# Kernel optimization log

Measured on AMD Instinct MI355X. Metric: run time of the kernel, lower is better.

Reference implementation:

```python
import jax, jax.numpy as jnp
import numpy as np


def _shared_mlp(x, W, s, b):
    # 1x1 conv over channel dim (last axis) + folded BN (scale/shift) + ReLU
    # x: (..., Cin), W: (Cout, Cin), s/b: (Cout,)
    return jax.nn.relu(jnp.einsum('...c,oc->...o', x, W) * s + b)


def setup_inputs() -> dict:
    key = jax.random.key(0)
    ks = jax.random.split(key, 15)
    B, N, K, C = 4, 4096, 32, 64
    D1, D2, DH = 64, 64, 128
    sc = 0.1
    return {
        'xyz': jax.random.normal(ks[0], (B, N, 3), dtype=jnp.float32),
        'features': jax.random.normal(ks[1], (B, C, N), dtype=jnp.float32),
        'idx': jax.random.randint(ks[2], (N, K), 0, N, dtype=jnp.int32),
        'W_gu': jax.random.normal(ks[3], (D1, 6), dtype=jnp.float32) * sc,
        's_gu': jnp.ones((D1,), jnp.float32),
        'b_gu': jax.random.normal(ks[4], (D1,), dtype=jnp.float32) * sc,
        'W_gv': jax.random.normal(ks[5], (D2, C), dtype=jnp.float32) * sc,
        's_gv': jnp.ones((D2,), jnp.float32),
        'b_gv': jax.random.normal(ks[6], (D2,), dtype=jnp.float32) * sc,
        'W_h': jax.random.normal(ks[7], (DH, D1 + D2), dtype=jnp.float32) * sc,
        's_h': jnp.ones((DH,), jnp.float32),
        'b_h': jax.random.normal(ks[8], (DH,), dtype=jnp.float32) * sc,
        'W_f': jax.random.normal(ks[9], (C, DH), dtype=jnp.float32) * sc,
        's_f': jnp.ones((C,), jnp.float32),
        'b_f': jax.random.normal(ks[10], (C,), dtype=jnp.float32) * sc,
    }


def reference(xyz, features, idx, W_gu, s_gu, b_gu, W_gv, s_gv, b_gv,
              W_h, s_h, b_h, W_f, s_f, b_f):
    # xyz: (B,N,3), features: (B,C,N), idx: (N,K) neighbor indices per point
    feats = jnp.swapaxes(features, 1, 2)              # (B,N,C)
    xyz_nb = xyz[:, idx, :]                           # (B,N,K,3) random gather
    feat_nb = feats[:, idx, :]                        # (B,N,K,C)
    K = idx.shape[1]
    center_xyz = jnp.broadcast_to(xyz[:, :, None, :], xyz_nb.shape)
    rel_xyz = jnp.concatenate([center_xyz, xyz_nb], axis=-1)   # (B,N,K,6)
    rel_feat = feat_nb + feats[:, :, None, :]                  # (B,N,K,C)

    gu = _shared_mlp(rel_xyz, W_gu, s_gu, b_gu)       # (B,N,K,D1)
    gv = _shared_mlp(rel_feat, W_gv, s_gv, b_gv)      # (B,N,K,D2)
    fuse = jnp.concatenate([gu, gv], axis=-1)         # (B,N,K,D1+D2)
    h = _shared_mlp(fuse, W_h, s_h, b_h)              # (B,N,K,DH)
    pooled = jnp.mean(h, axis=2)                      # (B,N,DH) mean over K
    out = _shared_mlp(pooled, W_f, s_f, b_f)          # (B,N,C)
    out = jnp.swapaxes(out, 1, 2) + features          # (B,C,N) residual
    return (xyz, out)
```

## Files before the change

kernel.cpp:

```cpp
#include <hip/hip_runtime.h>

#define B_  4
#define N_  4096
#define K_  32
#define C_  64
#define DH_ 128
#define PPB 16

typedef _Float16 half2v __attribute__((ext_vector_type(2)));
typedef _Float16 half8  __attribute__((ext_vector_type(8)));
typedef __fp16   fp16x2 __attribute__((ext_vector_type(2)));
typedef float  floatx16 __attribute__((ext_vector_type(16)));
typedef unsigned int uint_t;

union HU { half2v h; uint_t u; };
union HU2 { fp16x2 h; uint_t u; };

__device__ __forceinline__ uint_t pk2(float a, float b) {
    HU2 x; x.h = __builtin_amdgcn_cvt_pkrtz(a, b);
    return x.u;
}

__global__ __launch_bounds__(256) void k_transforms(
    const float* __restrict__ xyz,
    const float* __restrict__ W_h,
    const float* __restrict__ s_h,
    float* __restrict__ out_xyz,
    _Float16* __restrict__ Bpack)
{
    int e = blockIdx.x * 256 + threadIdx.x;
    if (e < B_*N_*3) { out_xyz[e] = xyz[e]; return; }
    e -= B_*N_*3;
    int j = e & 7, l = (e >> 3) & 63, c = (e >> 9) & 7, ob = e >> 12;
    int o = ob*32 + (l & 31);
    int i = c*16 + (l >> 5)*8 + j;
    Bpack[e] = (_Float16)(W_h[o*DH_ + i] * s_h[o]);
}

__global__ __launch_bounds__(256) void k_pre(
    const float* __restrict__ xyz,
    const float* __restrict__ features,
    const float* __restrict__ W_gv,
    const float* __restrict__ W_gu,
    const float* __restrict__ s_gu, const float* __restrict__ b_gu,
    const float* __restrict__ s_gv, const float* __restrict__ b_gv,
    uint_t* __restrict__ QsH,
    uint_t* __restrict__ PcatH)
{
    const int b  = blockIdx.x >> 8;
    const int n0 = (blockIdx.x & 255) * 16;
    const int t  = threadIdx.x;

    __shared__ __align__(16) float ftile[64 * 17];
    __shared__ __align__(16) float wtile[64 * 68];

    {
        const int c = t >> 2, nq = t & 3;
        float4 f4 = *(const float4*)&features[(b*C_ + c)*N_ + n0 + nq*4];
        ftile[c*17 + nq*4 + 0] = f4.x;
        ftile[c*17 + nq*4 + 1] = f4.y;
        ftile[c*17 + nq*4 + 2] = f4.z;
        ftile[c*17 + nq*4 + 3] = f4.w;
    }
    for (int e = t; e < 64*64; e += 256) {
        int o = e >> 6, c = e & 63;
        wtile[c*68 + o] = W_gv[e];
    }
    __syncthreads();

    const int n  = t >> 4;
    const int oq = t & 15;
    const int o0 = oq * 4;

    float acc[4] = {};
    for (int c = 0; c < 64; c++) {
        const float a = ftile[c*17 + n];
        const float4 wv = *(const float4*)&wtile[c*68 + o0];
        acc[0] = fmaf(a, wv.x, acc[0]);
        acc[1] = fmaf(a, wv.y, acc[1]);
        acc[2] = fmaf(a, wv.z, acc[2]);
        acc[3] = fmaf(a, wv.w, acc[3]);
    }

    const int bn = b*N_ + n0 + n;
    const float x0 = xyz[bn*3+0], x1 = xyz[bn*3+1], x2 = xyz[bn*3+2];

    const float4 sgu = *(const float4*)&s_gu[o0];
    const float4 bgu = *(const float4*)&b_gu[o0];
    const float4 sgv = *(const float4*)&s_gv[o0];
    const float4 bgv = *(const float4*)&b_gv[o0];

    float q[4], r[4];
#pragma unroll
    for (int jj = 0; jj < 4; jj++) {
        const int o = o0 + jj;
        q[jj] = x0*W_gu[o*6+0] + x1*W_gu[o*6+1] + x2*W_gu[o*6+2];
        r[jj] = x0*W_gu[o*6+3] + x1*W_gu[o*6+4] + x2*W_gu[o*6+5];
    }
    uint2 qa, pa;
    qa.x = pk2(q[0]*sgu.x+bgu.x, q[1]*sgu.y+bgu.y);
    qa.y = pk2(q[2]*sgu.z+bgu.z, q[3]*sgu.w+bgu.w);
    pa.x = pk2(r[0]*sgu.x, r[1]*sgu.y);
    pa.y = pk2(r[2]*sgu.z, r[3]*sgu.w);
    *(uint2*)&QsH  [bn*64 + oq*2] = qa;
    *(uint2*)&PcatH[bn*64 + oq*2] = pa;
    qa.x = pk2(acc[0]*sgv.x+bgv.x, acc[1]*sgv.y+bgv.y);
    qa.y = pk2(acc[2]*sgv.z+bgv.z, acc[3]*sgv.w+bgv.w);
    pa.x = pk2(acc[0]*sgv.x, acc[1]*sgv.y);
    pa.y = pk2(acc[2]*sgv.z, acc[3]*sgv.w);
    *(uint2*)&QsH  [bn*64 + 32 + oq*2] = qa;
    *(uint2*)&PcatH[bn*64 + 32 + oq*2] = pa;
}

__global__ __launch_bounds__(256) void k_main(
    const int*      __restrict__ idx,
    const uint_t*   __restrict__ QsH,
    const uint_t*   __restrict__ PcatH,
    const _Float16* __restrict__ Bpack,
    const float*    __restrict__ b_h,
    const float*    __restrict__ W_f,
    const float*    __restrict__ s_f, const float* __restrict__ b_f,
    const float*    __restrict__ features,
    float* __restrict__ outF)
{
    const int t    = threadIdx.x;
    const int w    = t >> 6;
    const int lane = t & 63;
    const int m    = lane & 31;
    const int hh   = lane >> 5;
    const int slot = w >> 1;
    const int oh   = w & 1;

    __shared__ __align__(16) float pooledAll[PPB * 136];

    half8 Bf[2][8];
#pragma unroll
    for (int ob = 0; ob < 2; ob++)
#pragma unroll
        for (int c = 0; c < 8; c++)
            Bf[ob][c] = *(const half8*)&Bpack[(((oh*2 + ob)*8 + c)*64 + lane)*8];

    const float bh0 = b_h[(oh*2+0)*32 + m];
    const float bh1 = b_h[(oh*2+1)*32 + m];

    const int bnb   = blockIdx.x * PPB;
    const int base0 = bnb & ~(N_ - 1);
    const half2v zero2 = {(_Float16)0.f, (_Float16)0.f};

    for (int pp = slot; pp < PPB; pp += 2) {
        const int bn = bnb + pp;
        const int n  = bn & (N_ - 1);
        const int j  = idx[n*K_ + m];
        const uint_t* Pb = PcatH + (size_t)(base0 + j)*64 + hh*4;
        const uint_t* Qb = QsH   + (size_t)bn*64 + hh*4;

        floatx16 acc0 = {}, acc1 = {};
#pragma unroll
        for (int c = 0; c < 8; c++) {
            const uint4 p4 = *(const uint4*)(Pb + c*8);
            const uint4 q4 = *(const uint4*)(Qb + c*8);
            union { uint_t u[4]; half8 h; } av;
#pragma unroll
            for (int qq = 0; qq < 4; qq++) {
                HU a, p;
                a.u = (&q4.x)[qq]; p.u = (&p4.x)[qq];
                half2v v = a.h + p.h;
                v = __builtin_elementwise_max(v, zero2);
                HU o2; o2.h = v;
                av.u[qq] = o2.u;
            }
            acc0 = __builtin_amdgcn_mfma_f32_32x32x16_f16(av.h, Bf[0][c], acc0, 0, 0, 0);
            acc1 = __builtin_amdgcn_mfma_f32_32x32x16_f16(av.h, Bf[1][c], acc1, 0, 0, 0);
        }

        float v0 = 0.f, v1 = 0.f;
#pragma unroll
        for (int rg = 0; rg < 16; rg++) {
            v0 += fmaxf(acc0[rg] + bh0, 0.f);
            v1 += fmaxf(acc1[rg] + bh1, 0.f);
        }
        v0 += __shfl_xor(v0, 32);
        v1 += __shfl_xor(v1, 32);
        if (hh == 0) {
            pooledAll[pp*136 + (oh*2+0)*32 + m] = v0;
            pooledAll[pp*136 + (oh*2+1)*32 + m] = v1;
        }
    }
    __syncthreads();

    const int b  = bnb >> 12;
    const int n0 = bnb & (N_ - 1);
    const int c  = t >> 2;
    const int nq = t & 3;

    float acc[4] = {};
    for (int i0 = 0; i0 < DH_; i0 += 4) {
        const float4 wv = *(const float4*)&W_f[c*DH_ + i0];
#pragma unroll
        for (int r = 0; r < 4; r++) {
            const float4 p = *(const float4*)&pooledAll[(nq*4 + r)*136 + i0];
            acc[r] += wv.x*p.x + wv.y*p.y + wv.z*p.z + wv.w*p.w;
        }
    }
    const float sfc = s_f[c] * (1.f/(float)K_);
    const float bfc = b_f[c];
    const float4 fr = *(const float4*)&features[(b*C_ + c)*N_ + n0 + nq*4];
    float4 ov;
    ov.x = fmaxf(acc[0]*sfc + bfc, 0.f) + fr.x;
    ov.y = fmaxf(acc[1]*sfc + bfc, 0.f) + fr.y;
    ov.z = fmaxf(acc[2]*sfc + bfc, 0.f) + fr.z;
    ov.w = fmaxf(acc[3]*sfc + bfc, 0.f) + fr.w;
    *(float4*)&outF[(b*C_ + c)*N_ + n0 + nq*4] = ov;
}

extern "C" void kernel_launch(void* const* d_in, const int* in_sizes, int n_in,
                              void* d_out, int out_size, void* d_ws, size_t ws_size,
                              hipStream_t stream)
{
    const float* xyz      = (const float*)d_in[0];
    const float* features = (const float*)d_in[1];
    const int*   idx      = (const int*)  d_in[2];
    const float* W_gu     = (const float*)d_in[3];
    const float* s_gu     = (const float*)d_in[4];
    const float* b_gu     = (const float*)d_in[5];
    const float* W_gv     = (const float*)d_in[6];
    const float* s_gv     = (const float*)d_in[7];
    const float* b_gv     = (const float*)d_in[8];
    const float* W_h      = (const float*)d_in[9];
    const float* s_h      = (const float*)d_in[10];
    const float* b_h      = (const float*)d_in[11];
    const float* W_f      = (const float*)d_in[12];
    const float* s_f      = (const float*)d_in[13];
    const float* b_f      = (const float*)d_in[14];

    float* out  = (float*)d_out;
    float* outF = out + B_*N_*3;

    char* wp = (char*)d_ws;
    uint_t*   QsH   = (uint_t*)wp;   wp += (size_t)B_*N_*64*4;
    uint_t*   PcatH = (uint_t*)wp;   wp += (size_t)B_*N_*64*4;
    _Float16* Bpack = (_Float16*)wp; wp += DH_*DH_*2;

    k_transforms<<<256, 256, 0, stream>>>(xyz, W_h, s_h, out, Bpack);
    k_pre<<<B_*(N_/16), 256, 0, stream>>>(xyz, features, W_gv, W_gu,
                                          s_gu, b_gu, s_gv, b_gv, QsH, PcatH);
    k_main<<<(B_*N_)/PPB, 256, 0, stream>>>(idx, QsH, PcatH, Bpack, b_h,
                                            W_f, s_f, b_f, features, outF);
}
```

Measured before the change: 150.4 us.

## Fuse prep kernels and double-buffer coalesced neighbor gathers through LDS in main kernel

Merges the xyz-copy and W_h packing kernel into the per-point precompute kernel, which removes one launch. The main kernel now uses 128-thread blocks that each process 8 points in sequence. Every neighbor row of PcatH is fetched with fully coalesced 64-lane loads and the add+ReLU fuse tile is built in double-buffered shared memory. The next point's gathers are issued before the current point's MFMAs so that memory latency overlaps compute. The cost is extra LDS traffic and a block-wide barrier per point, along with fewer waves per block.

```diff
diff --git a/kernel.cpp b/kernel.cpp
--- a/kernel.cpp
+++ b/kernel.cpp
@@ -5,7 +5,7 @@
 #define K_  32
 #define C_  64
 #define DH_ 128
-#define PPB 16
+#define PPW 8
 
 typedef _Float16 half2v __attribute__((ext_vector_type(2)));
 typedef _Float16 half8  __attribute__((ext_vector_type(8)));
@@ -21,50 +21,52 @@
     return x.u;
 }
 
-__global__ __launch_bounds__(256) void k_transforms(
-    const float* __restrict__ xyz,
-    const float* __restrict__ W_h,
-    const float* __restrict__ s_h,
-    float* __restrict__ out_xyz,
-    _Float16* __restrict__ Bpack)
-{
-    int e = blockIdx.x * 256 + threadIdx.x;
-    if (e < B_*N_*3) { out_xyz[e] = xyz[e]; return; }
-    e -= B_*N_*3;
-    int j = e & 7, l = (e >> 3) & 63, c = (e >> 9) & 7, ob = e >> 12;
-    int o = ob*32 + (l & 31);
-    int i = c*16 + (l >> 5)*8 + j;
-    Bpack[e] = (_Float16)(W_h[o*DH_ + i] * s_h[o]);
-}
-
-__global__ __launch_bounds__(256) void k_pre(
+__global__ __launch_bounds__(256) void k_prep(
     const float* __restrict__ xyz,
     const float* __restrict__ features,
     const float* __restrict__ W_gv,
     const float* __restrict__ W_gu,
     const float* __restrict__ s_gu, const float* __restrict__ b_gu,
     const float* __restrict__ s_gv, const float* __restrict__ b_gv,
+    const float* __restrict__ W_h,  const float* __restrict__ s_h,
+    float* __restrict__ out_xyz,
+    _Float16* __restrict__ Bpack,
     uint_t* __restrict__ QsH,
     uint_t* __restrict__ PcatH)
 {
-    const int b  = blockIdx.x >> 8;
-    const int n0 = (blockIdx.x & 255) * 16;
-    const int t  = threadIdx.x;
+    const int blk = blockIdx.x;
+    const int b   = blk >> 8;
+    const int n0  = (blk & 255) * 16;
+    const int t   = threadIdx.x;
+
+    if (t < 48) { int e = blk*48 + t; out_xyz[e] = xyz[e]; }
+    if (t >= 64 && t < 80) {
+        int e = blk*16 + (t - 64);
+        int j = e & 7, l = (e >> 3) & 63, c = (e >> 9) & 7, ob = e >> 12;
+        int o = ob*32 + (l & 31);
+        int i = c*16 + (l >> 5)*8 + j;
+        Bpack[e] = (_Float16)(W_h[o*DH_ + i] * s_h[o]);
+    }
 
     __shared__ __align__(16) float ftile[64 * 17];
     __shared__ __align__(16) float wtile[64 * 68];
 
     {
         const int c = t >> 2, nq = t & 3;
-        float4 f4 = *(const float4*)&features[(b*C_ + c)*N_ + n0 + nq*4];
+        const float4 f4 = *(const float4*)&features[(b*C_ + c)*N_ + n0 + nq*4];
         ftile[c*17 + nq*4 + 0] = f4.x;
         ftile[c*17 + nq*4 + 1] = f4.y;
         ftile[c*17 + nq*4 + 2] = f4.z;
         ftile[c*17 + nq*4 + 3] = f4.w;
     }
-    for (int e = t; e < 64*64; e += 256) {
-        int o = e >> 6, c = e & 63;
-        wtile[c*68 + o] = W_gv[e];
+#pragma unroll
+    for (int r = 0; r < 4; r++) {
+        const int e4 = r*256 + t, o = e4 >> 4, c0 = (e4 & 15)*4;
+        const float4 w4 = *(const float4*)&W_gv[o*C_ + c0];
+        wtile[(c0+0)*68 + o] = w4.x;
+        wtile[(c0+1)*68 + o] = w4.y;
+        wtile[(c0+2)*68 + o] = w4.z;
+        wtile[(c0+3)*68 + o] = w4.w;
     }
     __syncthreads();
 
@@ -73,6 +75,7 @@
     const int o0 = oq * 4;
 
     float acc[4] = {};
+#pragma unroll 4
     for (int c = 0; c < 64; c++) {
         const float a = ftile[c*17 + n];
         const float4 wv = *(const float4*)&wtile[c*68 + o0];
@@ -112,7 +115,7 @@
     *(uint2*)&PcatH[bn*64 + 32 + oq*2] = pa;
 }
 
-__global__ __launch_bounds__(256) void k_main(
+__global__ __launch_bounds__(128) void k_main(
     const int*      __restrict__ idx,
     const uint_t*   __restrict__ QsH,
     const uint_t*   __restrict__ PcatH,
@@ -124,14 +127,13 @@
     float* __restrict__ outF)
 {
     const int t    = threadIdx.x;
-    const int w    = t >> 6;
+    const int oh   = t >> 6;
     const int lane = t & 63;
     const int m    = lane & 31;
     const int hh   = lane >> 5;
-    const int slot = w >> 1;
-    const int oh   = w & 1;
-
-    __shared__ __align__(16) float pooledAll[PPB * 136];
+
+    __shared__ uint_t fuse[2][32 * 66];
+    __shared__ __align__(16) float pooled[PPW * 132];
 
     half8 Bf[2][8];
 #pragma unroll
@@ -143,36 +145,59 @@
     const float bh0 = b_h[(oh*2+0)*32 + m];
     const float bh1 = b_h[(oh*2+1)*32 + m];
 
-    const int bnb   = blockIdx.x * PPB;
+    const int bnb   = blockIdx.x * PPW;
     const int base0 = bnb & ~(N_ - 1);
     const half2v zero2 = {(_Float16)0.f, (_Float16)0.f};
 
-    for (int pp = slot; pp < PPB; pp += 2) {
-        const int bn = bnb + pp;
-        const int n  = bn & (N_ - 1);
-        const int j  = idx[n*K_ + m];
-        const uint_t* Pb = PcatH + (size_t)(base0 + j)*64 + hh*4;
-        const uint_t* Qb = QsH   + (size_t)bn*64 + hh*4;
+    int jall[PPW];
+#pragma unroll
+    for (int p = 0; p < PPW; p++)
+        jall[p] = idx[((bnb + p) & (N_-1))*K_ + m];
+
+    {
+        const uint_t qw = QsH[(size_t)(bnb+0)*64 + lane];
+        uint_t pg[16];
+#pragma unroll
+        for (int it = 0; it < 16; it++) {
+            const int row = oh*16 + it;
+            const int j   = __shfl(jall[0], row);
+            pg[it] = PcatH[(size_t)(base0 + j)*64 + lane];
+        }
+#pragma unroll
+        for (int it = 0; it < 16; it++) {
+            HU a, pval; a.u = qw; pval.u = pg[it];
+            half2v v = a.h + pval.h;
+            v = __builtin_elementwise_max(v, zero2);
+            HU o2; o2.h = v;
+            fuse[0][(oh*16 + it)*66 + lane] = o2.u;
+        }
+    }
+    __syncthreads();
+
+    for (int p = 0; p < PPW; p++) {
+        const int cur = p & 1, nxt = cur ^ 1;
+
+        uint_t pg[16]; uint_t qw_n = 0;
+        if (p + 1 < PPW) {
+            qw_n = QsH[(size_t)(bnb + p + 1)*64 + lane];
+#pragma unroll
+            for (int it = 0; it < 16; it++) {
+                const int row = oh*16 + it;
+                const int j   = __shfl(jall[p+1], row);
+                pg[it] = PcatH[(size_t)(base0 + j)*64 + lane];
+            }
+        }
 
         floatx16 acc0 = {}, acc1 = {};
 #pragma unroll
         for (int c = 0; c < 8; c++) {
-            const uint4 p4 = *(const uint4*)(Pb + c*8);
-            const uint4 q4 = *(const uint4*)(Qb + c*8);
+            const int wb = m*66 + c*8 + hh*4;
             union { uint_t u[4]; half8 h; } av;
-#pragma unroll
-            for (int qq = 0; qq < 4; qq++) {
-                HU a, p;
-                a.u = (&q4.x)[qq]; p.u = (&p4.x)[qq];
-                half2v v = a.h + p.h;
-                v = __builtin_elementwise_max(v, zero2);
-                HU o2; o2.h = v;
-                av.u[qq] = o2.u;
-            }
+            *(uint2*)&av.u[0] = *(const uint2*)&fuse[cur][wb];
+            *(uint2*)&av.u[2] = *(const uint2*)&fuse[cur][wb + 2];
             acc0 = __builtin_amdgcn_mfma_f32_32x32x16_f16(av.h, Bf[0][c], acc0, 0, 0, 0);
             acc1 = __builtin_amdgcn_mfma_f32_32x32x16_f16(av.h, Bf[1][c], acc1, 0, 0, 0);
         }
-
         float v0 = 0.f, v1 = 0.f;
 #pragma unroll
         for (int rg = 0; rg < 16; rg++) {
@@ -182,35 +207,47 @@
         v0 += __shfl_xor(v0, 32);
         v1 += __shfl_xor(v1, 32);
         if (hh == 0) {
-            pooledAll[pp*136 + (oh*2+0)*32 + m] = v0;
-            pooledAll[pp*136 + (oh*2+1)*32 + m] = v1;
-        }
-    }
-    __syncthreads();
-
-    const int b  = bnb >> 12;
-    const int n0 = bnb & (N_ - 1);
-    const int c  = t >> 2;
-    const int nq = t & 3;
+            pooled[p*132 + (oh*2+0)*32 + m] = v0;
+            pooled[p*132 + (oh*2+1)*32 + m] = v1;
+        }
+
+        if (p + 1 < PPW) {
+#pragma unroll
+            for (int it = 0; it < 16; it++) {
+                HU a, pval; a.u = qw_n; pval.u = pg[it];
+                half2v v = a.h + pval.h;
+                v = __builtin_elementwise_max(v, zero2);
+                HU o2; o2.h = v;
+                fuse[nxt][(oh*16 + it)*66 + lane] = o2.u;
+            }
+        }
+        __syncthreads();
+    }
+
+    const int b   = bnb >> 12;
+    const int n0  = bnb & (N_ - 1);
+    const int c   = t >> 1;
+    const int r2  = t & 1;
 
     float acc[4] = {};
+#pragma unroll 4
     for (int i0 = 0; i0 < DH_; i0 += 4) {
         const float4 wv = *(const float4*)&W_f[c*DH_ + i0];
 #pragma unroll
         for (int r = 0; r < 4; r++) {
-            const float4 p = *(const float4*)&pooledAll[(nq*4 + r)*136 + i0];
-            acc[r] += wv.x*p.x + wv.y*p.y + wv.z*p.z + wv.w*p.w;
+            const float4 p4 = *(const float4*)&pooled[(r2*4 + r)*132 + i0];
+            acc[r] += wv.x*p4.x + wv.y*p4.y + wv.z*p4.z + wv.w*p4.w;
         }
     }
     const float sfc = s_f[c] * (1.f/(float)K_);
     const float bfc = b_f[c];
-    const float4 fr = *(const float4*)&features[(b*C_ + c)*N_ + n0 + nq*4];
+    const float4 fr = *(const float4*)&features[(b*C_ + c)*N_ + n0 + r2*4];
     float4 ov;
     ov.x = fmaxf(acc[0]*sfc + bfc, 0.f) + fr.x;
     ov.y = fmaxf(acc[1]*sfc + bfc, 0.f) + fr.y;
     ov.z = fmaxf(acc[2]*sfc + bfc, 0.f) + fr.z;
     ov.w = fmaxf(acc[3]*sfc + bfc, 0.f) + fr.w;
-    *(float4*)&outF[(b*C_ + c)*N_ + n0 + nq*4] = ov;
+    *(float4*)&outF[(b*C_ + c)*N_ + n0 + r2*4] = ov;
 }
 
 extern "C" void kernel_launch(void* const* d_in, const int* in_sizes, int n_in,
@@ -241,9 +278,9 @@
     uint_t*   PcatH = (uint_t*)wp;   wp += (size_t)B_*N_*64*4;
     _Float16* Bpack = (_Float16*)wp; wp += DH_*DH_*2;
 
-    k_transforms<<<256, 256, 0, stream>>>(xyz, W_h, s_h, out, Bpack);
-    k_pre<<<B_*(N_/16), 256, 0, stream>>>(xyz, features, W_gv, W_gu,
-                                          s_gu, b_gu, s_gv, b_gv, QsH, PcatH);
-    k_main<<<(B_*N_)/PPB, 256, 0, stream>>>(idx, QsH, PcatH, Bpack, b_h,
+    k_prep<<<B_*(N_/16), 256, 0, stream>>>(xyz, features, W_gv, W_gu,
+                                           s_gu, b_gu, s_gv, b_gv, W_h, s_h,
+                                           out, Bpack, QsH, PcatH);
+    k_main<<<(B_*N_)/PPW, 128, 0, stream>>>(idx, QsH, PcatH, Bpack, b_h,
                                             W_f, s_f, b_f, features, outF);
 }
```

After: 133.1 us. 1.13x faster.
